# Performance work log

Hardware: AMD Instinct MI355X
Metric: run time of the kernel (lower is better)

## Reference

```python
import jax, jax.numpy as jnp
import numpy as np

H = 512; NH = 8; L = 2; NPRED = 26; MAXF = 5; FF = 4 * H


def _ln(x, w, b, eps=1e-5):
    m = x.mean(-1, keepdims=True)
    v = ((x - m) ** 2).mean(-1, keepdims=True)
    return (x - m) / jnp.sqrt(v + eps) * w + b


def _gelu(x):
    return jax.nn.gelu(x, approximate=False)


def _mha(q_in, kv_in, in_w, in_b, out_w, out_b, nh=NH):
    # PyTorch nn.MultiheadAttention math (batch_first), no mask, eval mode.
    h = q_in.shape[-1]; dh = h // nh
    Wq, Wk, Wv = in_w[:h], in_w[h:2 * h], in_w[2 * h:]
    bq, bk, bv = in_b[:h], in_b[h:2 * h], in_b[2 * h:]
    B, Tq, _ = q_in.shape
    Tk = kv_in.shape[1]
    q = (q_in @ Wq.T + bq).reshape(B, Tq, nh, dh)
    k = (kv_in @ Wk.T + bk).reshape(B, Tk, nh, dh)
    v = (kv_in @ Wv.T + bv).reshape(B, Tk, nh, dh)
    s = jnp.einsum('bqhd,bkhd->bhqk', q, k) / jnp.sqrt(jnp.asarray(dh, q.dtype))
    a = jax.nn.softmax(s, axis=-1)
    o = jnp.einsum('bhqk,bkhd->bqhd', a, v).reshape(B, Tq, h)
    return o @ out_w.T + out_b


def setup_inputs():
    key = jax.random.key(0)
    ks = iter(jax.random.split(key, 48))
    r = lambda *s: jax.random.normal(next(ks), s, jnp.float32) * 0.02
    inp = {
        'temporal_context': jax.random.normal(next(ks), (16, 10, H), jnp.float32),
        'object_features': jax.random.normal(next(ks), (16, 20, H), jnp.float32),
        'future_queries': r(MAXF, H),
        'sa_in_w': r(L, 3 * H, H), 'sa_in_b': jnp.zeros((L, 3 * H), jnp.float32),
        'sa_out_w': r(L, H, H), 'sa_out_b': jnp.zeros((L, H), jnp.float32),
        'ca_in_w': r(L, 3 * H, H), 'ca_in_b': jnp.zeros((L, 3 * H), jnp.float32),
        'ca_out_w': r(L, H, H), 'ca_out_b': jnp.zeros((L, H), jnp.float32),
        'ff1_w': r(L, FF, H), 'ff1_b': jnp.zeros((L, FF), jnp.float32),
        'ff2_w': r(L, H, FF), 'ff2_b': jnp.zeros((L, H), jnp.float32),
        'n1_w': jnp.ones((L, H), jnp.float32), 'n1_b': jnp.zeros((L, H), jnp.float32),
        'n2_w': jnp.ones((L, H), jnp.float32), 'n2_b': jnp.zeros((L, H), jnp.float32),
        'n3_w': jnp.ones((L, H), jnp.float32), 'n3_b': jnp.zeros((L, H), jnp.float32),
        'norm_w': jnp.ones((H,), jnp.float32), 'norm_b': jnp.zeros((H,), jnp.float32),
        'pe1_w': r(H, 3 * H), 'pe1_b': jnp.zeros((H,), jnp.float32),
        'pe2_w': r(H, H), 'pe2_b': jnp.zeros((H,), jnp.float32),
        'pred_w': r(NPRED, H), 'pred_b': jnp.zeros((NPRED,), jnp.float32),
        'ex_w': r(1, H), 'ex_b': jnp.zeros((1,), jnp.float32),
        'num_future_frames': 5,
    }
    return inp


def reference(temporal_context, object_features, future_queries, sa_in_w, sa_in_b,
              sa_out_w, sa_out_b, ca_in_w, ca_in_b, ca_out_w, ca_out_b,
              ff1_w, ff1_b, ff2_w, ff2_b, n1_w, n1_b, n2_w, n2_b, n3_w, n3_b,
              norm_w, norm_b, pe1_w, pe1_b, pe2_w, pe2_b, pred_w, pred_b,
              ex_w, ex_b, num_future_frames):
    B = temporal_context.shape[0]
    Fh = num_future_frames
    # Future queries expanded over batch -> TransformerDecoder (post-norm, gelu, eval)
    x = jnp.broadcast_to(future_queries[:Fh][None], (B, Fh, H))
    mem = temporal_context
    for l in range(L):
        x = _ln(x + _mha(x, x, sa_in_w[l], sa_in_b[l], sa_out_w[l], sa_out_b[l]), n1_w[l], n1_b[l])
        x = _ln(x + _mha(x, mem, ca_in_w[l], ca_in_b[l], ca_out_w[l], ca_out_b[l]), n2_w[l], n2_b[l])
        ff = _gelu(x @ ff1_w[l].T + ff1_b[l]) @ ff2_w[l].T + ff2_b[l]
        x = _ln(x + ff, n3_w[l], n3_b[l])
    ctx = _ln(x, norm_w, norm_b)  # (B, F, H)
    # Vectorized (i, j) pair construction, i != j, in the original loop order
    N = object_features.shape[1]
    ii, jj = np.nonzero(~np.eye(N, dtype=bool))  # row-major == for i: for j: skip i==j
    P = ii.shape[0]
    subj = object_features[:, ii]  # (B, P, H)
    obj = object_features[:, jj]   # (B, P, H)
    pair = jnp.concatenate([
        jnp.broadcast_to(subj[:, None], (B, Fh, P, H)),
        jnp.broadcast_to(obj[:, None], (B, Fh, P, H)),
        jnp.broadcast_to(ctx[:, :, None], (B, Fh, P, H)),
    ], axis=-1)  # (B, F, P, 3H)
    enc = _gelu(pair @ pe1_w.T + pe1_b) @ pe2_w.T + pe2_b  # (B, F, P, H)
    predicate_logits = enc @ pred_w.T + pred_b  # (B, F, P, 26)
    existence_logits = enc @ ex_w.T + ex_b      # (B, F, P, 1)
    return predicate_logits, existence_logits
```

## Files before the change

kernel.cpp:

```cpp
#include <hip/hip_runtime.h>
#include <math.h>

#define HD 512
#define FFD 2048
#define FH 5
#define TM 10
#define NO 20
#define NP 380
#define PRED_N 790400

#define XM_PLAIN 0
#define XM_GELU  1
#define XM_FQ    2
#define XM_LN    3
#define XM_LN2   4

typedef short bf16x8 __attribute__((ext_vector_type(8)));
typedef float floatx4 __attribute__((ext_vector_type(4)));

__device__ __forceinline__ float gelu_f(float v) {
    return 0.5f * v * (1.0f + erff(v * 0.70710678118654752440f));
}
__device__ __forceinline__ unsigned short f2bf(float x) {
    unsigned int u = __float_as_uint(x);
    u = (u + 0x7FFFu + ((u >> 16) & 1u)) >> 16;
    return (unsigned short)u;
}

template <int XMODE>
__device__ __forceinline__ void gemm_body(
    int bx, int by, int bz,
    const float* __restrict__ X, int ldx,
    const float* __restrict__ parts, int np, int pzstr,
    const float* __restrict__ bo,
    const float* __restrict__ lw, const float* __restrict__ lb,
    const float* __restrict__ fw, const float* __restrict__ fb,
    float* __restrict__ xout, int xmod, int gps,
    const float* __restrict__ W, int ldw,
    float* __restrict__ Y, int ldy, int zyoff,
    int Klen, float* lds)
{
    float* Wt = lds;
    float* Xs = lds + 8256;
    const int RT = (XMODE >= XM_LN) ? 8 : 16;
    int t = threadIdx.x;
    int nb = bx * 128;
    int r0 = by * RT;
    int kbase = bz * Klen;
    float* Yb = Y + (size_t)bz * zyoff;
    int c = t & 31, rg = t >> 5, scs = t >> 4, q = t & 15;

    if (XMODE >= XM_LN) {
        int rl = t >> 5;
        int r  = r0 + rl;
        int c0 = (t & 31) * 16;
        int rr = xmod ? (r % xmod) : r;
        float v[16];
        #pragma unroll
        for (int u = 0; u < 16; u += 4) {
            float4 a = *(const float4*)(X + (size_t)rr * ldx + c0 + u);
            float4 bb = *(const float4*)(bo + c0 + u);
            float vx = a.x + bb.x, vy = a.y + bb.y, vz = a.z + bb.z, vw = a.w + bb.w;
            for (int zz = 0; zz < np; ++zz) {
                float4 p = *(const float4*)(parts + (size_t)zz * pzstr + (size_t)r * HD + c0 + u);
                vx += p.x; vy += p.y; vz += p.z; vw += p.w;
            }
            v[u] = vx; v[u + 1] = vy; v[u + 2] = vz; v[u + 3] = vw;
        }
        float s1 = 0, s2 = 0;
        #pragma unroll
        for (int u = 0; u < 16; ++u) { s1 += v[u]; s2 += v[u] * v[u]; }
        #pragma unroll
        for (int o = 16; o > 0; o >>= 1) {
            s1 += __shfl_down(s1, o, 32);
            s2 += __shfl_down(s2, o, 32);
        }
        s1 = __shfl(s1, 0, 32); s2 = __shfl(s2, 0, 32);
        float mean = s1 * (1.0f / HD);
        float rstd = rsqrtf(s2 * (1.0f / HD) - mean * mean + 1e-5f);
        #pragma unroll
        for (int u = 0; u < 16; ++u)
            v[u] = (v[u] - mean) * rstd * lw[c0 + u] + lb[c0 + u];
        if (xout && bz == 0 && bx == 0) {
            #pragma unroll
            for (int u = 0; u < 16; u += 4)
                *(float4*)(xout + (size_t)r * HD + c0 + u) =
                    make_float4(v[u], v[u + 1], v[u + 2], v[u + 3]);
        }
        if (XMODE == XM_LN2) {
            float t1 = 0, t2 = 0;
            #pragma unroll
            for (int u = 0; u < 16; ++u) { t1 += v[u]; t2 += v[u] * v[u]; }
            #pragma unroll
            for (int o = 16; o > 0; o >>= 1) {
                t1 += __shfl_down(t1, o, 32);
                t2 += __shfl_down(t2, o, 32);
            }
            t1 = __shfl(t1, 0, 32); t2 = __shfl(t2, 0, 32);
            float m2 = t1 * (1.0f / HD);
            float rs2 = rsqrtf(t2 * (1.0f / HD) - m2 * m2 + 1e-5f);
            #pragma unroll
            for (int u = 0; u < 16; ++u)
                v[u] = (v[u] - m2) * rs2 * fw[c0 + u] + fb[c0 + u];
        }
        #pragma unroll
        for (int u = 0; u < 16; u += 4)
            *(float4*)(Xs + rl * HD + c0 + u) =
                make_float4(v[u], v[u + 1], v[u + 2], v[u + 3]);
        __syncthreads();
    }

    float a00 = 0, a01 = 0, a02 = 0, a03 = 0;
    float a10 = 0, a11 = 0, a12 = 0, a13 = 0;

    int nch = Klen >> 6;
    float4 wreg[8];
    float4 xra, xrb, xrc;
    {
        int kg = kbase;
        #pragma unroll
        for (int p = 0; p < 8; ++p)
            wreg[p] = *(const float4*)(W + (size_t)(nb + scs + p * 16) * ldw + kg + q * 4);
        if (XMODE == XM_PLAIN) {
            xra = *(const float4*)(X + (size_t)(r0 + scs) * ldx + kg + q * 4);
        } else if (XMODE == XM_FQ) {
            xra = *(const float4*)(X + (size_t)((r0 + scs) % FH) * ldx + kg + q * 4);
        } else if (XMODE == XM_GELU) {
            const float* p0 = X + (size_t)(r0 + scs) * ldx + kg + q * 4;
            xra = *(const float4*)p0;
            xrb = *(const float4*)(p0 + gps);
            xrc = *(const float4*)(bo + kg + q * 4);
        }
    }

    for (int ch = 0; ch < nch; ++ch) {
        if (ch) __syncthreads();
        if (XMODE <= XM_FQ) {
            float4 xv;
            if (XMODE == XM_GELU) {
                xv.x = gelu_f(xra.x + xrb.x + xrc.x);
                xv.y = gelu_f(xra.y + xrb.y + xrc.y);
                xv.z = gelu_f(xra.z + xrb.z + xrc.z);
                xv.w = gelu_f(xra.w + xrb.w + xrc.w);
            } else {
                xv = xra;
            }
            *(float4*)&Xs[scs * 64 + q * 4] = xv;
        }
        #pragma unroll
        for (int p = 0; p < 8; ++p) {
            int cc = scs + p * 16;
            Wt[(q * 4 + 0) * 129 + cc] = wreg[p].x;
            Wt[(q * 4 + 1) * 129 + cc] = wreg[p].y;
            Wt[(q * 4 + 2) * 129 + cc] = wreg[p].z;
            Wt[(q * 4 + 3) * 129 + cc] = wreg[p].w;
        }
        __syncthreads();
        if (ch + 1 < nch) {
            int kg = kbase + (ch + 1) * 64;
            #pragma unroll
            for (int p = 0; p < 8; ++p)
                wreg[p] = *(const float4*)(W + (size_t)(nb + scs + p * 16) * ldw + kg + q * 4);
            if (XMODE == XM_PLAIN) {
                xra = *(const float4*)(X + (size_t)(r0 + scs) * ldx + kg + q * 4);
            } else if (XMODE == XM_FQ) {
                xra = *(const float4*)(X + (size_t)((r0 + scs) % FH) * ldx + kg + q * 4);
            } else if (XMODE == XM_GELU) {
                const float* p0 = X + (size_t)(r0 + scs) * ldx + kg + q * 4;
                xra = *(const float4*)p0;
                xrb = *(const float4*)(p0 + gps);
                xrc = *(const float4*)(bo + kg + q * 4);
            }
        }
        if (RT == 16) {
            const float* xr0 = &Xs[(rg * 2 + 0) * 64];
            const float* xr1 = &Xs[(rg * 2 + 1) * 64];
            #pragma unroll
            for (int k4 = 0; k4 < 16; ++k4) {
                float4 x0 = *(const float4*)(xr0 + k4 * 4);
                float4 x1 = *(const float4*)(xr1 + k4 * 4);
                const float* x0p = (const float*)&x0;
                const float* x1p = (const float*)&x1;
                #pragma unroll
                for (int i = 0; i < 4; ++i) {
                    const float* wrow = &Wt[(k4 * 4 + i) * 129 + c];
                    float w0 = wrow[0], w1 = wrow[32], w2 = wrow[64], w3 = wrow[96];
                    float xi0 = x0p[i], xi1 = x1p[i];
                    a00 = fmaf(xi0, w0, a00); a01 = fmaf(xi0, w1, a01);
                    a02 = fmaf(xi0, w2, a02); a03 = fmaf(xi0, w3, a03);
                    a10 = fmaf(xi1, w0, a10); a11 = fmaf(xi1, w1, a11);
                    a12 = fmaf(xi1, w2, a12); a13 = fmaf(xi1, w3, a13);
                }
            }
        } else {
            const float* xr0 = &Xs[rg * HD + kbase + ch * 64];
            #pragma unroll
            for (int k4 = 0; k4 < 16; ++k4) {
                float4 x0 = *(const float4*)(xr0 + k4 * 4);
                const float* x0p = (const float*)&x0;
                #pragma unroll
                for (int i = 0; i < 4; ++i) {
                    const float* wrow = &Wt[(k4 * 4 + i) * 129 + c];
                    float xi0 = x0p[i];
                    a00 = fmaf(xi0, wrow[0],  a00);
                    a01 = fmaf(xi0, wrow[32], a01);
                    a02 = fmaf(xi0, wrow[64], a02);
                    a03 = fmaf(xi0, wrow[96], a03);
                }
            }
        }
    }
    if (RT == 16) {
        float* yr = Yb + (size_t)(r0 + rg * 2) * ldy + nb + c;
        yr[0] = a00; yr[32] = a01; yr[64] = a02; yr[96] = a03;
        yr += ldy;
        yr[0] = a10; yr[32] = a11; yr[64] = a12; yr[96] = a13;
    } else {
        float* yr = Yb + (size_t)(r0 + rg) * ldy + nb + c;
        yr[0] = a00; yr[32] = a01; yr[64] = a02; yr[96] = a03;
    }
}

template <int XMODE>
__global__ __launch_bounds__(256) void k_gemm(
    const float* __restrict__ X, int ldx,
    const float* __restrict__ parts, int np, int pzstr,
    const float* __restrict__ bo,
    const float* __restrict__ lw, const float* __restrict__ lb,
    const float* __restrict__ fw, const float* __restrict__ fb,
    float* __restrict__ xout, int xmod, int gps,
    const float* __restrict__ W, int ldw,
    float* __restrict__ Y, int ldy, int zyoff, int Klen)
{
    __shared__ float lds[(XMODE >= XM_LN) ? 12352 : 9280];
    gemm_body<XMODE>(blockIdx.x, blockIdx.y, blockIdx.z, X, ldx, parts, np, pzstr,
                     bo, lw, lb, fw, fb, xout, xmod, gps, W, ldw, Y, ldy, zyoff,
                     Klen, lds);
}

__device__ void mprep(int m, const float* __restrict__ pe2_w, const float* __restrict__ pe2_b,
                      const float* __restrict__ pred_w, const float* __restrict__ pred_b,
                      const float* __restrict__ ex_w, const float* __restrict__ ex_b,
                      unsigned short* __restrict__ Mbf, float* __restrict__ cb, float* lds)
{
    int t = threadIdx.x;
    if (m < 16) {
        int dl = t & 31, ec = t >> 5;
        int d = m * 32 + dl;
        float acc[27];
        #pragma unroll
        for (int k = 0; k < 27; ++k) acc[k] = 0.f;
        for (int sub = 0; sub < 2; ++sub) {
            __syncthreads();
            for (int idx = t; idx < 1728; idx += 256) {
                int g = idx / 216, r = idx - g * 216;
                int k = r >> 3, f4 = (r & 7) * 4;
                int eoff = g * 64 + sub * 32 + f4;
                float4 pv = (k < 26) ? *(const float4*)(pred_w + k * HD + eoff)
                                     : *(const float4*)(ex_w + eoff);
                *(float4*)(lds + g * 864 + k * 32 + f4) = pv;
            }
            __syncthreads();
            int ebase = ec * 64 + sub * 32;
            const float* ps = lds + ec * 864;
            #pragma unroll 2
            for (int e4 = 0; e4 < 8; ++e4) {
                float w0 = pe2_w[(size_t)(ebase + e4 * 4 + 0) * HD + d];
                float w1 = pe2_w[(size_t)(ebase + e4 * 4 + 1) * HD + d];
                float w2 = pe2_w[(size_t)(ebase + e4 * 4 + 2) * HD + d];
                float w3 = pe2_w[(size_t)(ebase + e4 * 4 + 3) * HD + d];
                #pragma unroll
                for (int k = 0; k < 27; ++k) {
                    float4 pv = *(const float4*)(ps + k * 32 + e4 * 4);
                    acc[k] += w0 * pv.x + w1 * pv.y + w2 * pv.z + w3 * pv.w;
                }
            }
        }
        __syncthreads();
        #pragma unroll
        for (int k = 0; k < 27; ++k) lds[(ec * 32 + dl) * 27 + k] = acc[k];
        __syncthreads();
        for (int idx = t; idx < 1024; idx += 256) {
            int dl2 = idx >> 5, k = idx & 31;
            float s = 0.f;
            if (k < 27) {
                #pragma unroll
                for (int e = 0; e < 8; ++e) s += lds[(e * 32 + dl2) * 27 + k];
            }
            int quad = dl2 >> 3, j = dl2 & 7;
            int nt = k >> 4, n15 = k & 15;
            int lane = quad * 16 + n15;
            Mbf[((size_t)(m * 2 + nt) * 64 + lane) * 8 + j] = f2bf(s);
        }
    } else {
        int g = t >> 3, li = t & 7;
        if (g < 27) {
            const float* wo = (g < 26) ? (pred_w + g * HD) : ex_w;
            float a = 0.f;
            for (int e = li; e < HD; e += 8) a += pe2_b[e] * wo[e];
            a += __shfl_down(a, 4, 8);
            a += __shfl_down(a, 2, 8);
            a += __shfl_down(a, 1, 8);
            if (li == 0) cb[g] = a + ((g < 26) ? pred_b[g] : ex_b[0]);
        }
    }
}

__global__ __launch_bounds__(256) void k_prep(
    const float* __restrict__ objf, const float* __restrict__ temporal,
    const float* __restrict__ fq,
    const float* __restrict__ pe1_w, const float* __restrict__ ca_in_w,
    const float* __restrict__ sa_in_w,
    const float* __restrict__ pe2_w, const float* __restrict__ pe2_b,
    const float* __restrict__ pred_w, const float* __restrict__ pred_b,
    const float* __restrict__ ex_w, const float* __restrict__ ex_b,
    float* __restrict__ SOp, float* __restrict__ kvb,
    float* __restrict__ qkvp,
    unsigned short* __restrict__ Mbf, float* __restrict__ cb)
{
    __shared__ float lds[9280];
    int blk = blockIdx.x;
    if (blk < 17) {
        mprep(blk, pe2_w, pe2_b, pred_w, pred_b, ex_w, ex_b, Mbf, cb, lds);
    } else if (blk < 337) {
        int s = blk - 17;
        int zw = s & 1, zk = (s >> 1) & 1, ct = (s >> 2) & 3, y = s >> 4;
        gemm_body<XM_PLAIN>(ct, y, zk, objf, HD, nullptr, 0, 0,
                            nullptr, nullptr, nullptr, nullptr, nullptr,
                            nullptr, 0, 0,
                            pe1_w + zw * 512, 1536,
                            SOp + zw * 512, 1024, 327680, 256, lds);
    } else if (blk < 657) {
        int s = blk - 337;
        int ct = s & 7, l = (s >> 3) & 1, zk = (s >> 4) & 1, y = s >> 5;
        gemm_body<XM_PLAIN>(ct, y, zk, temporal, HD, nullptr, 0, 0,
                            nullptr, nullptr, nullptr, nullptr, nullptr,
                            nullptr, 0, 0,
                            ca_in_w + (size_t)(l * 1536 + 512) * HD, HD,
                            kvb + (size_t)((zk * 2 + l) * 160) * 1024, 1024, 0, 256, lds);
    } else {
        int s = blk - 657;
        int x = s % 12, y = (s / 12) % 5, z = s / 60;
        gemm_body<XM_FQ>(x, y, z, fq, HD, nullptr, 0, 0,
                         nullptr, nullptr, nullptr, nullptr, nullptr,
                         nullptr, 0, 0,
                         sa_in_w, HD, qkvp, 1536, 122880, 128, lds);
    }
}

__global__ __launch_bounds__(256) void k_attnsa_proj(
    int l, const float* __restrict__ qkvp, const float* __restrict__ in_b,
    const float* __restrict__ Wout, float* __restrict__ yp)
{
    __shared__ float lds[8896];
    int bi = blockIdx.x;
    int b = bi >> 4, ct = (bi >> 2) & 3, zk = bi & 3;
    int t = threadIdx.x;
    float* qkv = lds;
    float* sc  = lds + 1920;
    float* aw  = lds + 1984;
    float* ao  = lds + 8256;
    float* Wt  = lds;
    int col0 = zk * 128;
    int c = t & 31, rg = t >> 5, scs = t >> 4, q = t & 15;
    int nb = ct * 128;

    float4 wreg[8];
    #pragma unroll
    for (int p = 0; p < 8; ++p)
        wreg[p] = *(const float4*)(Wout + (size_t)(nb + scs + p * 16) * HD + col0 + q * 4);

    for (int idx = t; idx < 480; idx += 256) {
        int m = idx / 160, r = idx - m * 160;
        int tok = r >> 5, c4 = (r & 31) * 4;
        int col = m * HD + col0 + c4;
        size_t o = (size_t)(b * FH + tok) * 1536 + col;
        float4 v = *(const float4*)(in_b + l * 1536 + col);
        #pragma unroll
        for (int z = 0; z < 4; ++z) {
            float4 p = *(const float4*)(qkvp + (size_t)z * 122880 + o);
            v.x += p.x; v.y += p.y; v.z += p.z; v.w += p.w;
        }
        *(float4*)(qkv + (m * FH + tok) * 128 + c4) = v;
    }
    __syncthreads();
    if (t < 50) {
        int hh = t / 25, r = t - hh * 25, tq = r / 5, tu = r % 5;
        float s = 0;
        for (int d = 0; d < 64; ++d)
            s += qkv[tq * 128 + hh * 64 + d] * qkv[(FH + tu) * 128 + hh * 64 + d];
        sc[t] = s * 0.125f;
    }
    __syncthreads();
    if (t < 10) {
        int base = (t / 5) * 25 + (t % 5) * 5;
        float mx = -1e30f;
        for (int u = 0; u < 5; ++u) mx = fmaxf(mx, sc[base + u]);
        float e[5], sm = 0;
        for (int u = 0; u < 5; ++u) { e[u] = expf(sc[base + u] - mx); sm += e[u]; }
        for (int u = 0; u < 5; ++u) aw[base + u] = e[u] / sm;
    }
    __syncthreads();
    for (int idx = t; idx < 640; idx += 256) {
        int tok = idx >> 7, cc = idx & 127, hh = cc >> 6;
        float s = 0;
        #pragma unroll
        for (int u = 0; u < 5; ++u)
            s += aw[hh * 25 + tok * 5 + u] * qkv[(2 * FH + u) * 128 + cc];
        ao[tok * 128 + cc] = s;
    }
    __syncthreads();

    float a0 = 0, a1 = 0, a2 = 0, a3 = 0;
    for (int ch = 0; ch < 2; ++ch) {
        if (ch) __syncthreads();
        #pragma unroll
        for (int p = 0; p < 8; ++p) {
            int cc = scs + p * 16;
            Wt[(q * 4 + 0) * 129 + cc] = wreg[p].x;
            Wt[(q * 4 + 1) * 129 + cc] = wreg[p].y;
            Wt[(q * 4 + 2) * 129 + cc] = wreg[p].z;
            Wt[(q * 4 + 3) * 129 + cc] = wreg[p].w;
        }
        __syncthreads();
        if (ch == 0) {
            #pragma unroll
            for (int p = 0; p < 8; ++p)
                wreg[p] = *(const float4*)(Wout + (size_t)(nb + scs + p * 16) * HD + col0 + 64 + q * 4);
        }
        if (rg < FH) {
            const float* xr = ao + rg * 128 + ch * 64;
            #pragma unroll
            for (int k4 = 0; k4 < 16; ++k4) {
                float4 xv = *(const float4*)(xr + k4 * 4);
                #pragma unroll
                for (int i = 0; i < 4; ++i) {
                    const float* wr = &Wt[(k4 * 4 + i) * 129 + c];
                    float x = ((const float*)&xv)[i];
                    a0 = fmaf(x, wr[0],  a0); a1 = fmaf(x, wr[32], a1);
                    a2 = fmaf(x, wr[64], a2); a3 = fmaf(x, wr[96], a3);
                }
            }
        }
    }
    if (rg < FH) {
        float* yr = yp + (size_t)zk * 40960 + (size_t)(b * FH + rg) * HD + nb + c;
        yr[0] = a0; yr[32] = a1; yr[64] = a2; yr[96] = a3;
    }
}

__global__ __launch_bounds__(256) void k_attnca_proj(
    int l, const float* __restrict__ qp, const float* __restrict__ kvb,
    const float* __restrict__ in_b, const float* __restrict__ Wout,
    float* __restrict__ yp)
{
    __shared__ float lds[8896];
    int bi = blockIdx.x;
    int b = bi >> 4, ct = (bi >> 2) & 3, zk = bi & 3;
    int t = threadIdx.x;
    float* qs = lds;
    float* kl = lds + 640;
    float* vl = lds + 1920;
    float* sc = lds + 3200;
    float* aw = lds + 3328;
    float* ao = lds + 8256;
    float* Wt = lds;
    const float* bb = in_b + l * 1536;
    int col0 = zk * 128;
    int c = t & 31, rg = t >> 5, scs = t >> 4, q = t & 15;
    int nb = ct * 128;

    float4 wreg[8];
    #pragma unroll
    for (int p = 0; p < 8; ++p)
        wreg[p] = *(const float4*)(Wout + (size_t)(nb + scs + p * 16) * HD + col0 + q * 4);

    if (t < 160) {
        int tok = t >> 5, c4 = (t & 31) * 4;
        size_t o = (size_t)(b * FH + tok) * HD + col0 + c4;
        float4 v = *(const float4*)(bb + col0 + c4);
        #pragma unroll
        for (int z = 0; z < 8; ++z) {
            float4 p = *(const float4*)(qp + (size_t)z * 40960 + o);
            v.x += p.x; v.y += p.y; v.z += p.z; v.w += p.w;
        }
        *(float4*)(qs + tok * 128 + c4) = v;
    }
    for (int idx = t; idx < 320; idx += 256) {
        int u = idx >> 5, c4 = (idx & 31) * 4;
        size_t base = (size_t)(l * 160 + b * TM + u) * 1024;
        float4 k0 = *(const float4*)(kvb + base + col0 + c4);
        float4 k1 = *(const float4*)(kvb + 327680 + base + col0 + c4);
        float4 bk = *(const float4*)(bb + 512 + col0 + c4);
        *(float4*)(kl + u * 128 + c4) =
            make_float4(k0.x + k1.x + bk.x, k0.y + k1.y + bk.y,
                        k0.z + k1.z + bk.z, k0.w + k1.w + bk.w);
        float4 v0 = *(const float4*)(kvb + base + 512 + col0 + c4);
        float4 v1 = *(const float4*)(kvb + 327680 + base + 512 + col0 + c4);
        float4 bv = *(const float4*)(bb + 1024 + col0 + c4);
        *(float4*)(vl + u * 128 + c4) =
            make_float4(v0.x + v1.x + bv.x, v0.y + v1.y + bv.y,
                        v0.z + v1.z + bv.z, v0.w + v1.w + bv.w);
    }
    __syncthreads();
    if (t < 100) {
        int hh = t / 50, r = t - hh * 50, tq = r / 10, tu = r % 10;
        float s = 0;
        for (int d = 0; d < 64; ++d)
            s += qs[tq * 128 + hh * 64 + d] * kl[tu * 128 + hh * 64 + d];
        sc[t] = s * 0.125f;
    }
    __syncthreads();
    if (t < 10) {
        int base = (t / 5) * 50 + (t % 5) * 10;
        float mx = -1e30f;
        for (int u = 0; u < TM; ++u) mx = fmaxf(mx, sc[base + u]);
        float e[TM], sm = 0;
        for (int u = 0; u < TM; ++u) { e[u] = expf(sc[base + u] - mx); sm += e[u]; }
        for (int u = 0; u < TM; ++u) aw[base + u] = e[u] / sm;
    }
    __syncthreads();
    for (int idx = t; idx < 640; idx += 256) {
        int tok = idx >> 7, cc = idx & 127, hh = cc >> 6;
        float s = 0;
        #pragma unroll
        for (int u = 0; u < TM; ++u)
            s += aw[hh * 50 + tok * 10 + u] * vl[u * 128 + cc];
        ao[tok * 128 + cc] = s;
    }
    __syncthreads();

    float a0 = 0, a1 = 0, a2 = 0, a3 = 0;
    for (int ch = 0; ch < 2; ++ch) {
        if (ch) __syncthreads();
        #pragma unroll
        for (int p = 0; p < 8; ++p) {
            int cc = scs + p * 16;
            Wt[(q * 4 + 0) * 129 + cc] = wreg[p].x;
            Wt[(q * 4 + 1) * 129 + cc] = wreg[p].y;
            Wt[(q * 4 + 2) * 129 + cc] = wreg[p].z;
            Wt[(q * 4 + 3) * 129 + cc] = wreg[p].w;
        }
        __syncthreads();
        if (ch == 0) {
            #pragma unroll
            for (int p = 0; p < 8; ++p)
                wreg[p] = *(const float4*)(Wout + (size_t)(nb + scs + p * 16) * HD + col0 + 64 + q * 4);
        }
        if (rg < FH) {
            const float* xr = ao + rg * 128 + ch * 64;
            #pragma unroll
            for (int k4 = 0; k4 < 16; ++k4) {
                float4 xv = *(const float4*)(xr + k4 * 4);
                #pragma unroll
                for (int i = 0; i < 4; ++i) {
                    const float* wr = &Wt[(k4 * 4 + i) * 129 + c];
                    float x = ((const float*)&xv)[i];
                    a0 = fmaf(x, wr[0],  a0); a1 = fmaf(x, wr[32], a1);
                    a2 = fmaf(x, wr[64], a2); a3 = fmaf(x, wr[96], a3);
                }
            }
        }
    }
    if (rg < FH) {
        float* yr = yp + (size_t)zk * 40960 + (size_t)(b * FH + rg) * HD + nb + c;
        yr[0] = a0; yr[32] = a1; yr[64] = a2; yr[96] = a3;
    }
}

__global__ __launch_bounds__(256) void k_pair(
    const float* __restrict__ SOp, const float* __restrict__ cpb,
    const float* __restrict__ pe1_b,
    const unsigned short* __restrict__ Mbf, const float* __restrict__ cb,
    float* __restrict__ out)
{
    __shared__ float lds[14964];
    int blk = blockIdx.x;
    int third = blk % 3, bf = blk / 3;
    int b = bf / FH, f = bf % FH;
    int t = threadIdx.x;
    int wv = t >> 6, lane = t & 63;
    int quad = lane >> 4, n15 = lane & 15;
    int i0 = (third == 0) ? 0 : (third == 1 ? 6 : 13);

    for (int idx = t; idx < 29 * 128; idx += 256) {
        int row = idx >> 7, c4 = (idx & 127) << 2;
        float4 v;
        if (row < 8) {
            int i = i0 + row; if (i > 19) i = 19;
            size_t o = (size_t)(b * NO + i) * 1024 + c4;
            float4 p0 = *(const float4*)(SOp + o);
            float4 p1 = *(const float4*)(SOp + 327680 + o);
            v = make_float4(p0.x + p1.x, p0.y + p1.y, p0.z + p1.z, p0.w + p1.w);
        } else if (row < 28) {
            int j = row - 8;
            size_t o = (size_t)(b * NO + j) * 1024 + 512 + c4;
            float4 p0 = *(const float4*)(SOp + o);
            float4 p1 = *(const float4*)(SOp + 327680 + o);
            v = make_float4(p0.x + p1.x, p0.y + p1.y, p0.z + p1.z, p0.w + p1.w);
        } else {
            size_t o = (size_t)(b * FH + f) * HD + c4;
            float4 s = *(const float4*)(cpb + o);
            #pragma unroll
            for (int z = 1; z < 8; ++z) {
                float4 p = *(const float4*)(cpb + (size_t)z * 40960 + o);
                s.x += p.x; s.y += p.y; s.z += p.z; s.w += p.w;
            }
            float4 pb = *(const float4*)(pe1_b + c4);
            v = make_float4(s.x + pb.x, s.y + pb.y, s.z + pb.z, s.w + pb.w);
        }
        *(float4*)(lds + row * 516 + c4) = v;
    }
    __syncthreads();

    floatx4 acc00 = {0,0,0,0}, acc01 = {0,0,0,0}, acc10 = {0,0,0,0}, acc11 = {0,0,0,0};
    for (int ks = 0; ks < 16; ++ks) {
        bf16x8 b0 = *(const bf16x8*)(Mbf + ((size_t)(ks * 2 + 0) * 64 + lane) * 8);
        bf16x8 b1 = *(const bf16x8*)(Mbf + ((size_t)(ks * 2 + 1) * 64 + lane) * 8);
        #pragma unroll
        for (int mt = 0; mt < 2; ++mt) {
            int p = third * 128 + wv * 32 + mt * 16 + n15;
            bf16x8 afr = {0, 0, 0, 0, 0, 0, 0, 0};
            if (p < NP) {
                int i = p / 19, j0 = p % 19;
                int j = j0 + (j0 >= i ? 1 : 0);
                int dof = ks * 32 + quad * 8;
                const float* Sr = lds + (i - i0) * 516 + dof;
                const float* Or = lds + (8 + j) * 516 + dof;
                const float* Cr = lds + 28 * 516 + dof;
                float4 sa = *(const float4*)Sr, sb = *(const float4*)(Sr + 4);
                float4 oa = *(const float4*)Or, ob = *(const float4*)(Or + 4);
                float4 ca = *(const float4*)Cr, cc = *(const float4*)(Cr + 4);
                union { unsigned short u[8]; bf16x8 v8; } pk;
                pk.u[0] = f2bf(gelu_f(sa.x + oa.x + ca.x));
                pk.u[1] = f2bf(gelu_f(sa.y + oa.y + ca.y));
                pk.u[2] = f2bf(gelu_f(sa.z + oa.z + ca.z));
                pk.u[3] = f2bf(gelu_f(sa.w + oa.w + ca.w));
                pk.u[4] = f2bf(gelu_f(sb.x + ob.x + cc.x));
                pk.u[5] = f2bf(gelu_f(sb.y + ob.y + cc.y));
                pk.u[6] = f2bf(gelu_f(sb.z + ob.z + cc.z));
                pk.u[7] = f2bf(gelu_f(sb.w + ob.w + cc.w));
                afr = pk.v8;
            }
            if (mt == 0) {
                acc00 = __builtin_amdgcn_mfma_f32_16x16x32_bf16(afr, b0, acc00, 0, 0, 0);
                acc01 = __builtin_amdgcn_mfma_f32_16x16x32_bf16(afr, b1, acc01, 0, 0, 0);
            } else {
                acc10 = __builtin_amdgcn_mfma_f32_16x16x32_bf16(afr, b0, acc10, 0, 0, 0);
                acc11 = __builtin_amdgcn_mfma_f32_16x16x32_bf16(afr, b1, acc11, 0, 0, 0);
            }
        }
    }
    int pbase = (b * FH + f) * NP;
    #pragma unroll
    for (int mt = 0; mt < 2; ++mt) {
        #pragma unroll
        for (int nt = 0; nt < 2; ++nt) {
            floatx4 a = (mt == 0) ? (nt == 0 ? acc00 : acc01)
                                  : (nt == 0 ? acc10 : acc11);
            int n = nt * 16 + n15;
            #pragma unroll
            for (int reg = 0; reg < 4; ++reg) {
                int p = third * 128 + wv * 32 + mt * 16 + quad * 4 + reg;
                if (p < NP && n < 27) {
                    float vout = a[reg] + cb[n];
                    if (n < 26) out[(size_t)(pbase + p) * 26 + n] = vout;
                    else        out[PRED_N + pbase + p] = vout;
                }
            }
        }
    }
}

extern "C" void kernel_launch(void* const* d_in, const int* in_sizes, int n_in,
                              void* d_out, int out_size, void* d_ws, size_t ws_size,
                              hipStream_t stream) {
    const float* temporal = (const float*)d_in[0];
    const float* objf     = (const float*)d_in[1];
    const float* fq       = (const float*)d_in[2];
    const float* sa_in_w  = (const float*)d_in[3];
    const float* sa_in_b  = (const float*)d_in[4];
    const float* sa_out_w = (const float*)d_in[5];
    const float* sa_out_b = (const float*)d_in[6];
    const float* ca_in_w  = (const float*)d_in[7];
    const float* ca_in_b  = (const float*)d_in[8];
    const float* ca_out_w = (const float*)d_in[9];
    const float* ca_out_b = (const float*)d_in[10];
    const float* ff1_w    = (const float*)d_in[11];
    const float* ff1_b    = (const float*)d_in[12];
    const float* ff2_w    = (const float*)d_in[13];
    const float* ff2_b    = (const float*)d_in[14];
    const float* n1_w     = (const float*)d_in[15];
    const float* n1_b     = (const float*)d_in[16];
    const float* n2_w     = (const float*)d_in[17];
    const float* n2_b     = (const float*)d_in[18];
    const float* n3_w     = (const float*)d_in[19];
    const float* n3_b     = (const float*)d_in[20];
    const float* norm_w   = (const float*)d_in[21];
    const float* norm_b   = (const float*)d_in[22];
    const float* pe1_w    = (const float*)d_in[23];
    const float* pe1_b    = (const float*)d_in[24];
    const float* pe2_w    = (const float*)d_in[25];
    const float* pe2_b    = (const float*)d_in[26];
    const float* pred_w   = (const float*)d_in[27];
    const float* pred_b   = (const float*)d_in[28];
    const float* ex_w     = (const float*)d_in[29];
    const float* ex_b     = (const float*)d_in[30];

    float* ws   = (float*)d_ws;
    float* x1   = ws;
    float* x2   = ws + 40960;
    float* x3   = ws + 81920;
    float* big  = ws + 122880;
    float* yp   = ws + 614400;
    float* kvb  = ws + 1269760;
    float* SOp  = ws + 1925120;
    float* cpb  = ws + 2580480;
    unsigned short* Mbf = (unsigned short*)(ws + 2908160);
    float* cb   = ws + 2916352;
    float* out  = (float*)d_out;
    float* qkvp = big;
    float* qp   = big;
    float* ffp  = big;

    k_prep<<<897, 256, 0, stream>>>(objf, temporal, fq, pe1_w, ca_in_w, sa_in_w,
                                    pe2_w, pe2_b, pred_w, pred_b, ex_w, ex_b,
                                    SOp, kvb, qkvp, Mbf, cb);
    for (int l = 0; l < 2; ++l) {
        if (l == 1) {
            k_gemm<XM_LN><<<dim3(12, 10, 4), 256, 0, stream>>>(
                x2, HD, yp, 16, 40960, ff2_b, n3_w, n3_b,
                nullptr, nullptr, x3, 0, 0,
                sa_in_w + 786432, HD, qkvp, 1536, 122880, 128);
        }
        k_attnsa_proj<<<256, 256, 0, stream>>>(l, qkvp, sa_in_b,
                                               sa_out_w + (size_t)l * 262144, yp);
        k_gemm<XM_LN><<<dim3(4, 10, 8), 256, 0, stream>>>(
            (l == 0 ? fq : x3), HD, yp, 4, 40960,
            sa_out_b + l * HD, n1_w + l * HD, n1_b + l * HD,
            nullptr, nullptr, x1, (l == 0 ? FH : 0), 0,
            ca_in_w + (size_t)l * 786432, HD, qp, HD, 40960, 64);
        k_attnca_proj<<<256, 256, 0, stream>>>(l, qp, kvb, ca_in_b,
                                               ca_out_w + (size_t)l * 262144, yp);
        k_gemm<XM_LN><<<dim3(16, 10, 2), 256, 0, stream>>>(
            x1, HD, yp, 4, 40960,
            ca_out_b + l * HD, n2_w + l * HD, n2_b + l * HD,
            nullptr, nullptr, x2, 0, 0,
            ff1_w + (size_t)l * 1048576, HD, ffp, FFD, 163840, 256);
        k_gemm<XM_GELU><<<dim3(4, 5, 16), 256, 0, stream>>>(
            ffp, FFD, nullptr, 0, 0, ff1_b + l * FFD,
            nullptr, nullptr, nullptr, nullptr, nullptr, 0, 163840,
            ff2_w + (size_t)l * 1048576, FFD, yp, HD, 40960, 128);
    }
    k_gemm<XM_LN2><<<dim3(4, 10, 8), 256, 0, stream>>>(
        x2, HD, yp, 16, 40960, ff2_b + HD, n3_w + HD, n3_b + HD,
        norm_w, norm_b, nullptr, 0, 0,
        pe1_w + 1024, 1536, cpb, HD, 40960, 64);
    k_pair<<<240, 256, 0, stream>>>(SOp, cpb, pe1_b, Mbf, cb, out);
}
```

Before: 368.3 us.

## Increase split-K for QKV and FF1 GEMMs and restructure pe2·pred precompute

Doubles the split-K factor for the layer-1 QKV GEMM (4→8) and the FF1 GEMM (2→4), halving K per block so more blocks run concurrently. Consumers are updated to sum the extra partials: attention sums a runtime count of partials and the GELU-input loader now sums four partial slices. The workspace is enlarged and buffers shifted to hold them. The prep kernel's pe2_w×pred_w fold is rewritten to stage both operands in LDS and give each thread four accumulators, replacing the 27-accumulator cross-warp reduction. The extra partial buffers add memory traffic and redundant reads of the LN inputs across split blocks.

```diff
diff --git a/kernel.cpp b/kernel.cpp
--- a/kernel.cpp
+++ b/kernel.cpp
@@ -115,7 +115,7 @@
 
     int nch = Klen >> 6;
     float4 wreg[8];
-    float4 xra, xrb, xrc;
+    float4 xra, xrb, xg2, xg3, xrc;
     {
         int kg = kbase;
         #pragma unroll
@@ -129,6 +129,8 @@
             const float* p0 = X + (size_t)(r0 + scs) * ldx + kg + q * 4;
             xra = *(const float4*)p0;
             xrb = *(const float4*)(p0 + gps);
+            xg2 = *(const float4*)(p0 + 2 * (size_t)gps);
+            xg3 = *(const float4*)(p0 + 3 * (size_t)gps);
             xrc = *(const float4*)(bo + kg + q * 4);
         }
     }
@@ -138,10 +140,10 @@
         if (XMODE <= XM_FQ) {
             float4 xv;
             if (XMODE == XM_GELU) {
-                xv.x = gelu_f(xra.x + xrb.x + xrc.x);
-                xv.y = gelu_f(xra.y + xrb.y + xrc.y);
-                xv.z = gelu_f(xra.z + xrb.z + xrc.z);
-                xv.w = gelu_f(xra.w + xrb.w + xrc.w);
+                xv.x = gelu_f(xra.x + xrb.x + xg2.x + xg3.x + xrc.x);
+                xv.y = gelu_f(xra.y + xrb.y + xg2.y + xg3.y + xrc.y);
+                xv.z = gelu_f(xra.z + xrb.z + xg2.z + xg3.z + xrc.z);
+                xv.w = gelu_f(xra.w + xrb.w + xg2.w + xg3.w + xrc.w);
             } else {
                 xv = xra;
             }
@@ -169,6 +171,8 @@
                 const float* p0 = X + (size_t)(r0 + scs) * ldx + kg + q * 4;
                 xra = *(const float4*)p0;
                 xrb = *(const float4*)(p0 + gps);
+                xg2 = *(const float4*)(p0 + 2 * (size_t)gps);
+                xg3 = *(const float4*)(p0 + 3 * (size_t)gps);
                 xrc = *(const float4*)(bo + kg + q * 4);
             }
         }
@@ -245,52 +249,42 @@
 {
     int t = threadIdx.x;
     if (m < 16) {
-        int dl = t & 31, ec = t >> 5;
+        int dl = t & 31, kg = t >> 5;
         int d = m * 32 + dl;
-        float acc[27];
-        #pragma unroll
-        for (int k = 0; k < 27; ++k) acc[k] = 0.f;
-        for (int sub = 0; sub < 2; ++sub) {
+        float* wstage = lds;
+        float* pstage = lds + 2048;
+        float acc0 = 0, acc1 = 0, acc2 = 0, acc3 = 0;
+        for (int ec = 0; ec < 8; ++ec) {
             __syncthreads();
-            for (int idx = t; idx < 1728; idx += 256) {
-                int g = idx / 216, r = idx - g * 216;
-                int k = r >> 3, f4 = (r & 7) * 4;
-                int eoff = g * 64 + sub * 32 + f4;
-                float4 pv = (k < 26) ? *(const float4*)(pred_w + k * HD + eoff)
-                                     : *(const float4*)(ex_w + eoff);
-                *(float4*)(lds + g * 864 + k * 32 + f4) = pv;
+            for (int idx = t; idx < 2048; idx += 256) {
+                int e = idx >> 5, k = idx & 31;
+                float wv = 0.f;
+                if (k < 26)      wv = pred_w[k * HD + ec * 64 + e];
+                else if (k == 26) wv = ex_w[ec * 64 + e];
+                wstage[e * 32 + k] = wv;
+                pstage[e * 32 + k] = pe2_w[(size_t)(ec * 64 + e) * HD + m * 32 + k];
             }
             __syncthreads();
-            int ebase = ec * 64 + sub * 32;
-            const float* ps = lds + ec * 864;
-            #pragma unroll 2
-            for (int e4 = 0; e4 < 8; ++e4) {
-                float w0 = pe2_w[(size_t)(ebase + e4 * 4 + 0) * HD + d];
-                float w1 = pe2_w[(size_t)(ebase + e4 * 4 + 1) * HD + d];
-                float w2 = pe2_w[(size_t)(ebase + e4 * 4 + 2) * HD + d];
-                float w3 = pe2_w[(size_t)(ebase + e4 * 4 + 3) * HD + d];
-                #pragma unroll
-                for (int k = 0; k < 27; ++k) {
-                    float4 pv = *(const float4*)(ps + k * 32 + e4 * 4);
-                    acc[k] += w0 * pv.x + w1 * pv.y + w2 * pv.z + w3 * pv.w;
-                }
-            }
-        }
-        __syncthreads();
-        #pragma unroll
-        for (int k = 0; k < 27; ++k) lds[(ec * 32 + dl) * 27 + k] = acc[k];
-        __syncthreads();
-        for (int idx = t; idx < 1024; idx += 256) {
-            int dl2 = idx >> 5, k = idx & 31;
-            float s = 0.f;
+            #pragma unroll 4
+            for (int e = 0; e < 64; ++e) {
+                float pw = pstage[e * 32 + dl];
+                float4 wv = *(const float4*)(wstage + e * 32 + kg * 4);
+                acc0 = fmaf(pw, wv.x, acc0);
+                acc1 = fmaf(pw, wv.y, acc1);
+                acc2 = fmaf(pw, wv.z, acc2);
+                acc3 = fmaf(pw, wv.w, acc3);
+            }
+        }
+        float accs[4] = {acc0, acc1, acc2, acc3};
+        int quad = dl >> 3, jj = dl & 7;
+        #pragma unroll
+        for (int j = 0; j < 4; ++j) {
+            int k = kg * 4 + j;
             if (k < 27) {
-                #pragma unroll
-                for (int e = 0; e < 8; ++e) s += lds[(e * 32 + dl2) * 27 + k];
-            }
-            int quad = dl2 >> 3, j = dl2 & 7;
-            int nt = k >> 4, n15 = k & 15;
-            int lane = quad * 16 + n15;
-            Mbf[((size_t)(m * 2 + nt) * 64 + lane) * 8 + j] = f2bf(s);
+                int nt = k >> 4, n15 = k & 15;
+                int lane = quad * 16 + n15;
+                Mbf[((size_t)(m * 2 + nt) * 64 + lane) * 8 + jj] = f2bf(accs[j]);
+            }
         }
     } else {
         int g = t >> 3, li = t & 7;
@@ -349,7 +343,7 @@
 }
 
 __global__ __launch_bounds__(256) void k_attnsa_proj(
-    int l, const float* __restrict__ qkvp, const float* __restrict__ in_b,
+    int l, int nzq, const float* __restrict__ qkvp, const float* __restrict__ in_b,
     const float* __restrict__ Wout, float* __restrict__ yp)
 {
     __shared__ float lds[8896];
@@ -376,8 +370,7 @@
         int col = m * HD + col0 + c4;
         size_t o = (size_t)(b * FH + tok) * 1536 + col;
         float4 v = *(const float4*)(in_b + l * 1536 + col);
-        #pragma unroll
-        for (int z = 0; z < 4; ++z) {
+        for (int z = 0; z < nzq; ++z) {
             float4 p = *(const float4*)(qkvp + (size_t)z * 122880 + o);
             v.x += p.x; v.y += p.y; v.z += p.z; v.w += p.w;
         }
@@ -712,12 +705,12 @@
     float* x2   = ws + 40960;
     float* x3   = ws + 81920;
     float* big  = ws + 122880;
-    float* yp   = ws + 614400;
-    float* kvb  = ws + 1269760;
-    float* SOp  = ws + 1925120;
-    float* cpb  = ws + 2580480;
-    unsigned short* Mbf = (unsigned short*)(ws + 2908160);
-    float* cb   = ws + 2916352;
+    float* yp   = ws + 1105920;
+    float* kvb  = ws + 1761280;
+    float* SOp  = ws + 2416640;
+    float* cpb  = ws + 3072000;
+    unsigned short* Mbf = (unsigned short*)(ws + 3399680);
+    float* cb   = ws + 3407872;
     float* out  = (float*)d_out;
     float* qkvp = big;
     float* qp   = big;
@@ -728,12 +721,12 @@
                                     SOp, kvb, qkvp, Mbf, cb);
     for (int l = 0; l < 2; ++l) {
         if (l == 1) {
-            k_gemm<XM_LN><<<dim3(12, 10, 4), 256, 0, stream>>>(
+            k_gemm<XM_LN><<<dim3(12, 10, 8), 256, 0, stream>>>(
                 x2, HD, yp, 16, 40960, ff2_b, n3_w, n3_b,
                 nullptr, nullptr, x3, 0, 0,
-                sa_in_w + 786432, HD, qkvp, 1536, 122880, 128);
-        }
-        k_attnsa_proj<<<256, 256, 0, stream>>>(l, qkvp, sa_in_b,
+                sa_in_w + 786432, HD, qkvp, 1536, 122880, 64);
+        }
+        k_attnsa_proj<<<256, 256, 0, stream>>>(l, (l == 0 ? 4 : 8), qkvp, sa_in_b,
                                                sa_out_w + (size_t)l * 262144, yp);
         k_gemm<XM_LN><<<dim3(4, 10, 8), 256, 0, stream>>>(
             (l == 0 ? fq : x3), HD, yp, 4, 40960,
@@ -742,11 +735,11 @@
             ca_in_w + (size_t)l * 786432, HD, qp, HD, 40960, 64);
         k_attnca_proj<<<256, 256, 0, stream>>>(l, qp, kvb, ca_in_b,
                                                ca_out_w + (size_t)l * 262144, yp);
-        k_gemm<XM_LN><<<dim3(16, 10, 2), 256, 0, stream>>>(
+        k_gemm<XM_LN><<<dim3(16, 10, 4), 256, 0, stream>>>(
             x1, HD, yp, 4, 40960,
             ca_out_b + l * HD, n2_w + l * HD, n2_b + l * HD,
             nullptr, nullptr, x2, 0, 0,
-            ff1_w + (size_t)l * 1048576, HD, ffp, FFD, 163840, 256);
+            ff1_w + (size_t)l * 1048576, HD, ffp, FFD, 163840, 128);
         k_gemm<XM_GELU><<<dim3(4, 5, 16), 256, 0, stream>>>(
             ffp, FFD, nullptr, 0, 0, ff1_b + l * FFD,
             nullptr, nullptr, nullptr, nullptr, nullptr, 0, 163840,
```

Result: slower. 394.2 us (+7.0%).
